# Kernel optimization log

Measured on AMD Instinct MI355X. Metric: run time of the kernel, lower is better.

## Reference

```python
import jax, jax.numpy as jnp
import numpy as np

OUT_F, IN_F, BLOCK, RANK = 8192, 8192, 32, 16
B, S = 4, 256
Q_ZERO = 128.0      # symmetric int8-style zero point for the Q8_0-like quants
LORA_SCALE = 2.0    # patch alpha applied by the patch function


def setup_inputs() -> dict:
    key = jax.random.key(0)
    k1, k2, k3, k4, k5, k6 = jax.random.split(key, 6)
    x = jax.random.normal(k1, (B, S, IN_F), dtype=jnp.float32)
    # block-quantized weight: int quants in [0,256) and per-block scales
    q_int = jax.random.randint(k2, (OUT_F, IN_F // BLOCK, BLOCK), 0, 256, dtype=jnp.int32)
    scales = jax.random.uniform(k3, (OUT_F, IN_F // BLOCK), dtype=jnp.float32) * 0.02
    lora_A = jax.random.normal(k4, (RANK, IN_F), dtype=jnp.float32) * 0.02
    lora_B = jax.random.normal(k5, (OUT_F, RANK), dtype=jnp.float32) * 0.02
    bias = jax.random.normal(k6, (OUT_F,), dtype=jnp.float32)
    return {"x": x, "q_int": q_int, "scales": scales,
            "lora_A": lora_A, "lora_B": lora_B, "bias": bias}


def reference(x, q_int, scales, lora_A, lora_B, bias):
    # --- get_weight(): dequantize GGML block-quantized tensor ---
    # w[o, b, e] = (q[o, b, e] - 128) * scale[o, b]
    w = (q_int.astype(jnp.float32) - Q_ZERO) * scales[:, :, None]   # [out, in//BLOCK, BLOCK]
    w = w.reshape(OUT_F, IN_F)                                      # [out, in]
    # --- apply patch function (LoRA add) ---
    w = w + LORA_SCALE * (lora_B @ lora_A)                          # [out, in]
    # --- cast_bias_weight + F.linear ---
    w = w.astype(x.dtype)
    y = jnp.einsum('bsi,oi->bso', x, w) + bias.astype(x.dtype)      # [B, S, out]
    return y
```

## Files before the change

kernel.cpp:

```cpp
#include <hip/hip_runtime.h>
#include <hip/hip_bf16.h>
#include <stdint.h>

#define OUT_F 8192
#define IN_F  8192
#define RANK  16
#define M_TOT 1024
#define BM 128
#define BN 128
#define BK 64
#define NK (IN_F / BK)
#define SCB (IN_F / 32)

typedef __bf16 bf16x8 __attribute__((ext_vector_type(8)));
typedef float  f32x4  __attribute__((ext_vector_type(4)));

static __device__ __forceinline__ uint32_t pack_bf16(float lo, float hi) {
    uint32_t a = __builtin_bit_cast(uint32_t, lo);
    uint32_t b = __builtin_bit_cast(uint32_t, hi);
    return ((a + 0x8000u) >> 16) | ((b + 0x8000u) & 0xffff0000u);
}

__global__ __launch_bounds__(256) void prep_kernel(
    const float* __restrict__ x, const int* __restrict__ q,
    uint2* __restrict__ xb2, uint32_t* __restrict__ qu32,
    float* __restrict__ t)
{
    const int gid = blockIdx.x * 256 + threadIdx.x;
    if (gid < M_TOT * RANK) t[gid] = 0.f;

    const float4* x4 = (const float4*)x;
#pragma unroll
    for (int j = 0; j < 4; ++j) {
        const int i = gid + j * 524288;
        const float4 v = x4[i];
        uint2 p;
        p.x = pack_bf16(v.x, v.y);
        p.y = pack_bf16(v.z, v.w);
        xb2[i] = p;
    }

    const int4* q4 = (const int4*)q;
#pragma unroll 8
    for (int k = 0; k < 32; ++k) {
        const size_t i = (size_t)gid + (size_t)k * 524288;
        const int4 a = q4[i];
        qu32[i] = (uint32_t)a.x | ((uint32_t)a.y << 8) |
                  ((uint32_t)a.z << 16) | ((uint32_t)a.w << 24);
    }
}

__global__ __launch_bounds__(256) void convert_kernel(
    const float* __restrict__ x, uint2* __restrict__ xb2, float* __restrict__ t)
{
    const int tid = threadIdx.x, b = blockIdx.x;
    if (b < 64) t[b * 256 + tid] = 0.f;
    const float4* x4 = (const float4*)x;
    const int base = b * 256 + tid;
#pragma unroll
    for (int j = 0; j < 8; ++j) {
        const int i = base + j * 262144;
        const float4 v = x4[i];
        uint2 p;
        p.x = pack_bf16(v.x, v.y);
        p.y = pack_bf16(v.z, v.w);
        xb2[i] = p;
    }
}

__global__ __launch_bounds__(256) void lora_t_kernel(
    const uint16_t* __restrict__ xb, const float* __restrict__ lora_A,
    float* __restrict__ t)
{
    const int b = blockIdx.x;
    const int mt = b >> 6, ks = b & 63;
    const int tid = threadIdx.x, wave = tid >> 6, lane = tid & 63;
    const int fr = lane & 15, quad = lane >> 4;
    const int m = mt * 64 + wave * 16 + fr;
    const int k0 = ks * 128 + quad * 8;

    f32x4 acc = {0.f, 0.f, 0.f, 0.f};
    const uint16_t* xr = xb + (size_t)m * IN_F + k0;
    const float* ar = lora_A + (size_t)fr * IN_F + k0;

#pragma unroll
    for (int s = 0; s < 4; ++s) {
        const bf16x8 af = *(const bf16x8*)(xr + s * 32);
        const float4 a0 = *(const float4*)(ar + s * 32);
        const float4 a1 = *(const float4*)(ar + s * 32 + 4);
        bf16x8 bfr;
        uint32_t* bp = (uint32_t*)&bfr;
        bp[0] = pack_bf16(a0.x, a0.y); bp[1] = pack_bf16(a0.z, a0.w);
        bp[2] = pack_bf16(a1.x, a1.y); bp[3] = pack_bf16(a1.z, a1.w);
        acc = __builtin_amdgcn_mfma_f32_16x16x32_bf16(af, bfr, acc, 0, 0, 0);
    }
    const int mout = mt * 64 + wave * 16 + quad * 4;
#pragma unroll
    for (int r = 0; r < 4; ++r)
        atomicAdd(&t[(size_t)(mout + r) * RANK + fr], acc[r]);
}

#define GEMM_STEP_U(KT, P, CUR, NXT)                                           \
    {                                                                          \
        const int ktn = ((KT) + 2) & (NK - 1);                                 \
        _Pragma("unroll")                                                      \
        for (int j = 0; j < 8; ++j) {                                          \
            const int row = qrow + 16 * j;                                     \
            qv[(P) ^ 1][j] = *(const uint32_t*)(qbase + (size_t)row * IN_F + ktn * BK); \
            sc[(P) ^ 1][j] = scales[(size_t)(n0 + row) * SCB + ktn * 2 + qhi]; \
        }                                                                      \
        const int kta = ((KT) + 1) & (NK - 1);                                 \
        _Pragma("unroll")                                                      \
        for (int i = 0; i < 4; ++i) {                                          \
            __builtin_amdgcn_global_load_lds(                                  \
                (const __attribute__((address_space(1))) uint32_t*)(xsrc + (size_t)kta * BK + (size_t)i * 8 * IN_F), \
                (__attribute__((address_space(3))) uint32_t*)(&xs[NXT][(wave * 32 + i * 8) * BK]), \
                16, 0, 0);                                                     \
        }                                                                      \
        _Pragma("unroll")                                                      \
        for (int j = 0; j < 8; ++j) {                                          \
            const float s = sc[P][j];                                          \
            const float c = -128.f * s;                                        \
            const uint32_t qq = qv[P][j];                                      \
            uint2 pk;                                                          \
            pk.x = pack_bf16(fmaf((float)(qq & 0xffu), s, c),                  \
                             fmaf((float)((qq >> 8) & 0xffu), s, c));          \
            pk.y = pack_bf16(fmaf((float)((qq >> 16) & 0xffu), s, c),          \
                             fmaf((float)(qq >> 24), s, c));                   \
            *(uint2*)(&wt[NXT][(qrow + 16 * j) * BK + wpos]) = pk;             \
        }                                                                      \
        _Pragma("unroll")                                                      \
        for (int kk = 0; kk < BK; kk += 32) {                                  \
            bf16x8 af[4], bfr[4];                                              \
            const int pp = (((kk >> 3) + quad) ^ (fr & 7)) * 8;                \
            _Pragma("unroll")                                                  \
            for (int i = 0; i < 4; ++i)                                        \
                af[i] = *(const bf16x8*)(&xs[CUR][(wm * 64 + i * 16 + fr) * BK + pp]); \
            _Pragma("unroll")                                                  \
            for (int j = 0; j < 4; ++j)                                        \
                bfr[j] = *(const bf16x8*)(&wt[CUR][(wn * 64 + j * 16 + fr) * BK + pp]); \
            _Pragma("unroll")                                                  \
            for (int i = 0; i < 4; ++i)                                        \
                _Pragma("unroll")                                              \
                for (int j = 0; j < 4; ++j)                                    \
                    acc[i][j] = __builtin_amdgcn_mfma_f32_16x16x32_bf16(af[i], bfr[j], acc[i][j], 0, 0, 0); \
        }                                                                      \
        __syncthreads();                                                       \
    }

__global__ __launch_bounds__(256, 2) void gemm_u8_kernel(
    const uint16_t* __restrict__ xb,
    const uint8_t*  __restrict__ qu8,
    const float*    __restrict__ scales,
    const float*    __restrict__ t,
    const float*    __restrict__ loraB,
    const float*    __restrict__ bias,
    float*          __restrict__ out)
{
    __shared__ __align__(16) uint16_t xs[2][BM * BK];
    __shared__ __align__(16) uint16_t wt[2][BN * BK];

    const int bx    = blockIdx.x;
    const int mtile = bx >> 6;
    const int ntile = bx & 63;
    const int m0 = mtile * BM;
    const int n0 = ntile * BN;

    const int tid  = threadIdx.x;
    const int wave = tid >> 6;
    const int lane = tid & 63;
    const int wm = wave & 1, wn = wave >> 1;
    const int fr = lane & 15;
    const int quad = lane >> 4;

    const int qrow  = tid >> 4;
    const int qcol4 = (tid & 15) * 4;
    const int qhi   = (tid >> 3) & 1;
    const int wpos = ((((tid >> 1) & 7) ^ (qrow & 7)) * 8) + (tid & 1) * 4;

    const uint8_t* qbase = qu8 + (size_t)n0 * IN_F + qcol4;

    f32x4 acc[4][4];
    const f32x4 z = {0.f, 0.f, 0.f, 0.f};
#pragma unroll
    for (int i = 0; i < 4; ++i)
#pragma unroll
        for (int j = 0; j < 4; ++j) acc[i][j] = z;

    uint32_t qv[2][8];
    float    sc[2][8];

#pragma unroll
    for (int j = 0; j < 8; ++j) {
        const int row = qrow + 16 * j;
        qv[0][j] = *(const uint32_t*)(qbase + (size_t)row * IN_F);
        sc[0][j] = scales[(size_t)(n0 + row) * SCB + qhi];
    }

    {
        if (tid < 128) {
            const int row = tid, s = row & 7;
            const float4* tp = (const float4*)(t + (size_t)(m0 + row) * RANK);
            const float4 v0 = tp[0], v1 = tp[1], v2 = tp[2], v3 = tp[3];
            uint32_t vals[8];
            vals[0] = pack_bf16(v0.x, v0.y); vals[1] = pack_bf16(v0.z, v0.w);
            vals[2] = pack_bf16(v1.x, v1.y); vals[3] = pack_bf16(v1.z, v1.w);
            vals[4] = pack_bf16(v2.x, v2.y); vals[5] = pack_bf16(v2.z, v2.w);
            vals[6] = pack_bf16(v3.x, v3.y); vals[7] = pack_bf16(v3.z, v3.w);
            uint32_t* dst = (uint32_t*)(&xs[0][row * BK]);
#pragma unroll
            for (int c = 0; c < 8; ++c) {
                const int p = (c ^ s) * 4;
                if (c < 2) {
                    dst[p + 0] = vals[c * 4 + 0]; dst[p + 1] = vals[c * 4 + 1];
                    dst[p + 2] = vals[c * 4 + 2]; dst[p + 3] = vals[c * 4 + 3];
                } else {
                    dst[p + 0] = 0; dst[p + 1] = 0; dst[p + 2] = 0; dst[p + 3] = 0;
                }
            }
        } else {
            const int row = tid - 128, s = row & 7;
            const float4* bp = (const float4*)(loraB + (size_t)(n0 + row) * RANK);
            const float4 v0 = bp[0], v1 = bp[1], v2 = bp[2], v3 = bp[3];
            uint32_t vals[8];
            vals[0] = pack_bf16(2.f * v0.x, 2.f * v0.y); vals[1] = pack_bf16(2.f * v0.z, 2.f * v0.w);
            vals[2] = pack_bf16(2.f * v1.x, 2.f * v1.y); vals[3] = pack_bf16(2.f * v1.z, 2.f * v1.w);
            vals[4] = pack_bf16(2.f * v2.x, 2.f * v2.y); vals[5] = pack_bf16(2.f * v2.z, 2.f * v2.w);
            vals[6] = pack_bf16(2.f * v3.x, 2.f * v3.y); vals[7] = pack_bf16(2.f * v3.z, 2.f * v3.w);
            uint32_t* dst = (uint32_t*)(&wt[0][row * BK]);
#pragma unroll
            for (int c = 0; c < 8; ++c) {
                const int p = (c ^ s) * 4;
                if (c < 2) {
                    dst[p + 0] = vals[c * 4 + 0]; dst[p + 1] = vals[c * 4 + 1];
                    dst[p + 2] = vals[c * 4 + 2]; dst[p + 3] = vals[c * 4 + 3];
                } else {
                    dst[p + 0] = 0; dst[p + 1] = 0; dst[p + 2] = 0; dst[p + 3] = 0;
                }
            }
        }
        __syncthreads();
        const int pp = (quad ^ (fr & 7)) * 8;
        bf16x8 af[4], bfr[4];
#pragma unroll
        for (int i = 0; i < 4; ++i)
            af[i] = *(const bf16x8*)(&xs[0][(wm * 64 + i * 16 + fr) * BK + pp]);
#pragma unroll
        for (int j = 0; j < 4; ++j)
            bfr[j] = *(const bf16x8*)(&wt[0][(wn * 64 + j * 16 + fr) * BK + pp]);
#pragma unroll
        for (int i = 0; i < 4; ++i)
#pragma unroll
            for (int j = 0; j < 4; ++j)
                acc[i][j] = __builtin_amdgcn_mfma_f32_16x16x32_bf16(af[i], bfr[j], acc[i][j], 0, 0, 0);
        __syncthreads();
    }

    const int xrow   = wave * 32 + (lane >> 3);
    const int xchunk = (lane & 7) ^ (lane >> 3);
    const uint16_t* xsrc = xb + (size_t)(m0 + xrow) * IN_F + xchunk * 8;

#pragma unroll
    for (int i = 0; i < 4; ++i) {
        __builtin_amdgcn_global_load_lds(
            (const __attribute__((address_space(1))) uint32_t*)(xsrc + (size_t)i * 8 * IN_F),
            (__attribute__((address_space(3))) uint32_t*)(&xs[0][(wave * 32 + i * 8) * BK]),
            16, 0, 0);
    }
#pragma unroll
    for (int j = 0; j < 8; ++j) {
        const float s = sc[0][j];
        const float c = -128.f * s;
        const uint32_t qq = qv[0][j];
        uint2 pk;
        pk.x = pack_bf16(fmaf((float)(qq & 0xffu), s, c),
                         fmaf((float)((qq >> 8) & 0xffu), s, c));
        pk.y = pack_bf16(fmaf((float)((qq >> 16) & 0xffu), s, c),
                         fmaf((float)(qq >> 24), s, c));
        *(uint2*)(&wt[0][(qrow + 16 * j) * BK + wpos]) = pk;
    }
#pragma unroll
    for (int j = 0; j < 8; ++j) {
        const int row = qrow + 16 * j;
        qv[0][j] = *(const uint32_t*)(qbase + (size_t)row * IN_F + 1 * BK);
        sc[0][j] = scales[(size_t)(n0 + row) * SCB + 2 + qhi];
    }
    __syncthreads();

    for (int kt = 0; kt < NK; kt += 2) {
        GEMM_STEP_U(kt,     0, 0, 1);
        GEMM_STEP_U(kt + 1, 1, 1, 0);
    }

#pragma unroll
    for (int j = 0; j < 4; ++j) {
        const int col = n0 + wn * 64 + j * 16 + fr;
        const float bv = bias[col];
#pragma unroll
        for (int i = 0; i < 4; ++i) {
            const int rbase = m0 + wm * 64 + i * 16 + quad * 4;
#pragma unroll
            for (int r = 0; r < 4; ++r)
                out[(size_t)(rbase + r) * OUT_F + col] = acc[i][j][r] + bv;
        }
    }
}

#define GEMM_STEP_L(KT, P, CUR, NXT)                                           \
    {                                                                          \
        const int ktn = ((KT) + 2) & (NK - 1);                                 \
        _Pragma("unroll")                                                      \
        for (int j = 0; j < 8; ++j) {                                          \
            const int row = qrow + 16 * j;                                     \
            qv[(P) ^ 1][j] = *(const int4*)(qbase + (size_t)row * IN_F + ktn * BK); \
            sc[(P) ^ 1][j] = scales[(size_t)(n0 + row) * SCB + ktn * 2 + qhi]; \
        }                                                                      \
        const int kta = ((KT) + 1) & (NK - 1);                                 \
        _Pragma("unroll")                                                      \
        for (int i = 0; i < 4; ++i) {                                          \
            __builtin_amdgcn_global_load_lds(                                  \
                (const __attribute__((address_space(1))) uint32_t*)(xsrc + (size_t)kta * BK + (size_t)i * 8 * IN_F), \
                (__attribute__((address_space(3))) uint32_t*)(&xs[NXT][(wave * 32 + i * 8) * BK]), \
                16, 0, 0);                                                     \
        }                                                                      \
        _Pragma("unroll")                                                      \
        for (int j = 0; j < 8; ++j) {                                          \
            const float s = sc[P][j];                                          \
            const float c = -128.f * s;                                        \
            const int4 qq = qv[P][j];                                          \
            uint2 pk;                                                          \
            pk.x = pack_bf16(fmaf((float)qq.x, s, c), fmaf((float)qq.y, s, c)); \
            pk.y = pack_bf16(fmaf((float)qq.z, s, c), fmaf((float)qq.w, s, c)); \
            *(uint2*)(&wt[NXT][(qrow + 16 * j) * BK + wpos]) = pk;             \
        }                                                                      \
        _Pragma("unroll")                                                      \
        for (int kk = 0; kk < BK; kk += 32) {                                  \
            bf16x8 af[4], bfr[4];                                              \
            const int pp = (((kk >> 3) + quad) ^ (fr & 7)) * 8;                \
            _Pragma("unroll")                                                  \
            for (int i = 0; i < 4; ++i)                                        \
                af[i] = *(const bf16x8*)(&xs[CUR][(wm * 64 + i * 16 + fr) * BK + pp]); \
            _Pragma("unroll")                                                  \
            for (int j = 0; j < 4; ++j)                                        \
                bfr[j] = *(const bf16x8*)(&wt[CUR][(wn * 64 + j * 16 + fr) * BK + pp]); \
            _Pragma("unroll")                                                  \
            for (int i = 0; i < 4; ++i)                                        \
                _Pragma("unroll")                                              \
                for (int j = 0; j < 4; ++j)                                    \
                    acc[i][j] = __builtin_amdgcn_mfma_f32_16x16x32_bf16(af[i], bfr[j], acc[i][j], 0, 0, 0); \
        }                                                                      \
        __syncthreads();                                                       \
    }

__global__ __launch_bounds__(256, 2) void gemm_kernel(
    const uint16_t* __restrict__ xb,
    const int*      __restrict__ q,
    const float*    __restrict__ scales,
    const float*    __restrict__ t,
    const float*    __restrict__ loraB,
    const float*    __restrict__ bias,
    float*          __restrict__ out)
{
    __shared__ __align__(16) uint16_t xs[2][BM * BK];
    __shared__ __align__(16) uint16_t wt[2][BN * BK];

    const int bx    = blockIdx.x;
    const int mtile = bx >> 6;
    const int ntile = bx & 63;
    const int m0 = mtile * BM;
    const int n0 = ntile * BN;

    const int tid  = threadIdx.x;
    const int wave = tid >> 6;
    const int lane = tid & 63;
    const int wm = wave & 1, wn = wave >> 1;
    const int fr = lane & 15;
    const int quad = lane >> 4;

    const int qrow  = tid >> 4;
    const int qcol4 = (tid & 15) * 4;
    const int qhi   = (tid >> 3) & 1;
    const int wpos = ((((tid >> 1) & 7) ^ (qrow & 7)) * 8) + (tid & 1) * 4;

    const int* qbase = q + (size_t)n0 * IN_F + qcol4;

    f32x4 acc[4][4];
    const f32x4 z = {0.f, 0.f, 0.f, 0.f};
#pragma unroll
    for (int i = 0; i < 4; ++i)
#pragma unroll
        for (int j = 0; j < 4; ++j) acc[i][j] = z;

    int4  qv[2][8];
    float sc[2][8];

#pragma unroll
    for (int j = 0; j < 8; ++j) {
        const int row = qrow + 16 * j;
        qv[0][j] = *(const int4*)(qbase + (size_t)row * IN_F);
        sc[0][j] = scales[(size_t)(n0 + row) * SCB + qhi];
    }

    {
        if (tid < 128) {
            const int row = tid, s = row & 7;
            const float4* tp = (const float4*)(t + (size_t)(m0 + row) * RANK);
            const float4 v0 = tp[0], v1 = tp[1], v2 = tp[2], v3 = tp[3];
            uint32_t vals[8];
            vals[0] = pack_bf16(v0.x, v0.y); vals[1] = pack_bf16(v0.z, v0.w);
            vals[2] = pack_bf16(v1.x, v1.y); vals[3] = pack_bf16(v1.z, v1.w);
            vals[4] = pack_bf16(v2.x, v2.y); vals[5] = pack_bf16(v2.z, v2.w);
            vals[6] = pack_bf16(v3.x, v3.y); vals[7] = pack_bf16(v3.z, v3.w);
            uint32_t* dst = (uint32_t*)(&xs[0][row * BK]);
#pragma unroll
            for (int c = 0; c < 8; ++c) {
                const int p = (c ^ s) * 4;
                if (c < 2) {
                    dst[p + 0] = vals[c * 4 + 0]; dst[p + 1] = vals[c * 4 + 1];
                    dst[p + 2] = vals[c * 4 + 2]; dst[p + 3] = vals[c * 4 + 3];
                } else {
                    dst[p + 0] = 0; dst[p + 1] = 0; dst[p + 2] = 0; dst[p + 3] = 0;
                }
            }
        } else {
            const int row = tid - 128, s = row & 7;
            const float4* bp = (const float4*)(loraB + (size_t)(n0 + row) * RANK);
            const float4 v0 = bp[0], v1 = bp[1], v2 = bp[2], v3 = bp[3];
            uint32_t vals[8];
            vals[0] = pack_bf16(2.f * v0.x, 2.f * v0.y); vals[1] = pack_bf16(2.f * v0.z, 2.f * v0.w);
            vals[2] = pack_bf16(2.f * v1.x, 2.f * v1.y); vals[3] = pack_bf16(2.f * v1.z, 2.f * v1.w);
            vals[4] = pack_bf16(2.f * v2.x, 2.f * v2.y); vals[5] = pack_bf16(2.f * v2.z, 2.f * v2.w);
            vals[6] = pack_bf16(2.f * v3.x, 2.f * v3.y); vals[7] = pack_bf16(2.f * v3.z, 2.f * v3.w);
            uint32_t* dst = (uint32_t*)(&wt[0][row * BK]);
#pragma unroll
            for (int c = 0; c < 8; ++c) {
                const int p = (c ^ s) * 4;
                if (c < 2) {
                    dst[p + 0] = vals[c * 4 + 0]; dst[p + 1] = vals[c * 4 + 1];
                    dst[p + 2] = vals[c * 4 + 2]; dst[p + 3] = vals[c * 4 + 3];
                } else {
                    dst[p + 0] = 0; dst[p + 1] = 0; dst[p + 2] = 0; dst[p + 3] = 0;
                }
            }
        }
        __syncthreads();
        const int pp = (quad ^ (fr & 7)) * 8;
        bf16x8 af[4], bfr[4];
#pragma unroll
        for (int i = 0; i < 4; ++i)
            af[i] = *(const bf16x8*)(&xs[0][(wm * 64 + i * 16 + fr) * BK + pp]);
#pragma unroll
        for (int j = 0; j < 4; ++j)
            bfr[j] = *(const bf16x8*)(&wt[0][(wn * 64 + j * 16 + fr) * BK + pp]);
#pragma unroll
        for (int i = 0; i < 4; ++i)
#pragma unroll
            for (int j = 0; j < 4; ++j)
                acc[i][j] = __builtin_amdgcn_mfma_f32_16x16x32_bf16(af[i], bfr[j], acc[i][j], 0, 0, 0);
        __syncthreads();
    }

    const int xrow   = wave * 32 + (lane >> 3);
    const int xchunk = (lane & 7) ^ (lane >> 3);
    const uint16_t* xsrc = xb + (size_t)(m0 + xrow) * IN_F + xchunk * 8;

#pragma unroll
    for (int i = 0; i < 4; ++i) {
        __builtin_amdgcn_global_load_lds(
            (const __attribute__((address_space(1))) uint32_t*)(xsrc + (size_t)i * 8 * IN_F),
            (__attribute__((address_space(3))) uint32_t*)(&xs[0][(wave * 32 + i * 8) * BK]),
            16, 0, 0);
    }
#pragma unroll
    for (int j = 0; j < 8; ++j) {
        const float s = sc[0][j];
        const float c = -128.f * s;
        const int4 qq = qv[0][j];
        uint2 pk;
        pk.x = pack_bf16(fmaf((float)qq.x, s, c), fmaf((float)qq.y, s, c));
        pk.y = pack_bf16(fmaf((float)qq.z, s, c), fmaf((float)qq.w, s, c));
        *(uint2*)(&wt[0][(qrow + 16 * j) * BK + wpos]) = pk;
    }
#pragma unroll
    for (int j = 0; j < 8; ++j) {
        const int row = qrow + 16 * j;
        qv[0][j] = *(const int4*)(qbase + (size_t)row * IN_F + 1 * BK);
        sc[0][j] = scales[(size_t)(n0 + row) * SCB + 2 + qhi];
    }
    __syncthreads();

    for (int kt = 0; kt < NK; kt += 2) {
        GEMM_STEP_L(kt,     0, 0, 1);
        GEMM_STEP_L(kt + 1, 1, 1, 0);
    }

#pragma unroll
    for (int j = 0; j < 4; ++j) {
        const int col = n0 + wn * 64 + j * 16 + fr;
        const float bv = bias[col];
#pragma unroll
        for (int i = 0; i < 4; ++i) {
            const int rbase = m0 + wm * 64 + i * 16 + quad * 4;
#pragma unroll
            for (int r = 0; r < 4; ++r)
                out[(size_t)(rbase + r) * OUT_F + col] = acc[i][j][r] + bv;
        }
    }
}

extern "C" void kernel_launch(void* const* d_in, const int* in_sizes, int n_in,
                              void* d_out, int out_size, void* d_ws, size_t ws_size,
                              hipStream_t stream) {
    const float* x      = (const float*)d_in[0];
    const int*   q      = (const int*)d_in[1];
    const float* scales = (const float*)d_in[2];
    const float* lora_A = (const float*)d_in[3];
    const float* lora_B = (const float*)d_in[4];
    const float* bias   = (const float*)d_in[5];
    float* out = (float*)d_out;

    const size_t xb_bytes = (size_t)M_TOT * IN_F * sizeof(uint16_t);
    const size_t t_bytes  = (size_t)M_TOT * RANK * sizeof(float);
    const size_t q8_off   = xb_bytes + t_bytes;
    const size_t q8_bytes = (size_t)OUT_F * IN_F;

    uint16_t* xb = (uint16_t*)d_ws;
    float*    t  = (float*)((char*)d_ws + xb_bytes);

    if (ws_size >= q8_off + q8_bytes) {
        uint8_t* qu8 = (uint8_t*)d_ws + q8_off;
        prep_kernel<<<2048, 256, 0, stream>>>(x, q, (uint2*)xb, (uint32_t*)qu8, t);
        lora_t_kernel<<<1024, 256, 0, stream>>>(xb, lora_A, t);
        gemm_u8_kernel<<<(M_TOT / BM) * (OUT_F / BN), 256, 0, stream>>>(
            xb, qu8, scales, t, lora_B, bias, out);
    } else {
        convert_kernel<<<M_TOT, 256, 0, stream>>>(x, (uint2*)xb, t);
        lora_t_kernel<<<1024, 256, 0, stream>>>(xb, lora_A, t);
        gemm_kernel<<<(M_TOT / BM) * (OUT_F / BN), 256, 0, stream>>>(
            xb, q, scales, t, lora_B, bias, out);
    }
}
```

Baseline: 602.3 us.

## Split K in two with single-buffered LDS, higher occupancy, and a reduce kernel

Adds a split-K GEMM that gives each of 1024 workgroups half of the K range and writes fp32 partial tiles to a workspace buffer. A separate reduce kernel then adds the two partials and the bias. The new kernel uses single-buffered LDS with launch bounds of 4 blocks per CU, trading the double-buffered pipeline for more resident waves and a 1024-block grid on the CUs. The cost is an extra 64 MB of partial traffic plus a reduce pass. It also drops the old int32 fallback path and needs a larger workspace to take the new path.

```diff
diff --git a/kernel.cpp b/kernel.cpp
--- a/kernel.cpp
+++ b/kernel.cpp
@@ -98,6 +98,207 @@
 #pragma unroll
     for (int r = 0; r < 4; ++r)
         atomicAdd(&t[(size_t)(mout + r) * RANK + fr], acc[r]);
+}
+
+#define GEMM_STEP_S(KT, KTN, P)                                                \
+    {                                                                          \
+        _Pragma("unroll")                                                      \
+        for (int i = 0; i < 4; ++i) {                                          \
+            __builtin_amdgcn_global_load_lds(                                  \
+                (const __attribute__((address_space(1))) uint32_t*)(xsrc + (size_t)(KT) * BK + (size_t)i * 8 * IN_F), \
+                (__attribute__((address_space(3))) uint32_t*)(&xs[(wave * 32 + i * 8) * BK]), \
+                16, 0, 0);                                                     \
+        }                                                                      \
+        _Pragma("unroll")                                                      \
+        for (int j = 0; j < 8; ++j) {                                          \
+            const float s = sc[P][j];                                          \
+            const float c = -128.f * s;                                        \
+            const uint32_t qq = qv[P][j];                                      \
+            uint2 pk;                                                          \
+            pk.x = pack_bf16(fmaf((float)(qq & 0xffu), s, c),                  \
+                             fmaf((float)((qq >> 8) & 0xffu), s, c));          \
+            pk.y = pack_bf16(fmaf((float)((qq >> 16) & 0xffu), s, c),          \
+                             fmaf((float)(qq >> 24), s, c));                   \
+            *(uint2*)(&wt[(qrow + 16 * j) * BK + wpos]) = pk;                  \
+        }                                                                      \
+        _Pragma("unroll")                                                      \
+        for (int j = 0; j < 8; ++j) {                                          \
+            const int row = qrow + 16 * j;                                     \
+            qv[(P) ^ 1][j] = *(const uint32_t*)(qbase + (size_t)row * IN_F + (size_t)(KTN) * BK); \
+            sc[(P) ^ 1][j] = scales[(size_t)(n0 + row) * SCB + (KTN) * 2 + qhi]; \
+        }                                                                      \
+        __syncthreads();   \
+        _Pragma("unroll")                                                      \
+        for (int kk = 0; kk < BK; kk += 32) {                                  \
+            bf16x8 af[4], bfr[4];                                              \
+            const int pp = (((kk >> 3) + quad) ^ (fr & 7)) * 8;                \
+            _Pragma("unroll")                                                  \
+            for (int i = 0; i < 4; ++i)                                        \
+                af[i] = *(const bf16x8*)(&xs[(wm * 64 + i * 16 + fr) * BK + pp]); \
+            _Pragma("unroll")                                                  \
+            for (int j = 0; j < 4; ++j)                                        \
+                bfr[j] = *(const bf16x8*)(&wt[(wn * 64 + j * 16 + fr) * BK + pp]); \
+            _Pragma("unroll")                                                  \
+            for (int i = 0; i < 4; ++i)                                        \
+                _Pragma("unroll")                                              \
+                for (int j = 0; j < 4; ++j)                                    \
+                    acc[i][j] = __builtin_amdgcn_mfma_f32_16x16x32_bf16(af[i], bfr[j], acc[i][j], 0, 0, 0); \
+        }                                                                      \
+        __syncthreads();                       \
+    }
+
+__global__ __launch_bounds__(256, 4) void gemm_u8s_kernel(
+    const uint16_t* __restrict__ xb,
+    const uint8_t*  __restrict__ qu8,
+    const float*    __restrict__ scales,
+    const float*    __restrict__ t,
+    const float*    __restrict__ loraB,
+    float*          __restrict__ part)
+{
+    __shared__ __align__(16) uint16_t xs[BM * BK];
+    __shared__ __align__(16) uint16_t wt[BN * BK];
+
+    const int bx    = blockIdx.x;
+    const int ks    = bx >> 9;
+    const int mtile = (bx >> 6) & 7;
+    const int ntile = bx & 63;
+    const int m0 = mtile * BM;
+    const int n0 = ntile * BN;
+    const int k0 = ks * (NK / 2);
+
+    const int tid  = threadIdx.x;
+    const int wave = tid >> 6;
+    const int lane = tid & 63;
+    const int wm = wave & 1, wn = wave >> 1;
+    const int fr = lane & 15;
+    const int quad = lane >> 4;
+
+    const int qrow  = tid >> 4;
+    const int qcol4 = (tid & 15) * 4;
+    const int qhi   = (tid >> 3) & 1;
+    const int wpos = ((((tid >> 1) & 7) ^ (qrow & 7)) * 8) + (tid & 1) * 4;
+
+    const uint8_t* qbase = qu8 + (size_t)n0 * IN_F + qcol4;
+
+    f32x4 acc[4][4];
+    const f32x4 z = {0.f, 0.f, 0.f, 0.f};
+#pragma unroll
+    for (int i = 0; i < 4; ++i)
+#pragma unroll
+        for (int j = 0; j < 4; ++j) acc[i][j] = z;
+
+    uint32_t qv[2][8];
+    float    sc[2][8];
+
+#pragma unroll
+    for (int j = 0; j < 8; ++j) {
+        const int row = qrow + 16 * j;
+        qv[0][j] = *(const uint32_t*)(qbase + (size_t)row * IN_F + (size_t)k0 * BK);
+        sc[0][j] = scales[(size_t)(n0 + row) * SCB + k0 * 2 + qhi];
+    }
+
+    if (ks == 0) {
+        if (tid < 128) {
+            const int row = tid, s = row & 7;
+            const float4* tp = (const float4*)(t + (size_t)(m0 + row) * RANK);
+            const float4 v0 = tp[0], v1 = tp[1], v2 = tp[2], v3 = tp[3];
+            uint32_t vals[8];
+            vals[0] = pack_bf16(v0.x, v0.y); vals[1] = pack_bf16(v0.z, v0.w);
+            vals[2] = pack_bf16(v1.x, v1.y); vals[3] = pack_bf16(v1.z, v1.w);
+            vals[4] = pack_bf16(v2.x, v2.y); vals[5] = pack_bf16(v2.z, v2.w);
+            vals[6] = pack_bf16(v3.x, v3.y); vals[7] = pack_bf16(v3.z, v3.w);
+            uint32_t* dst = (uint32_t*)(&xs[row * BK]);
+#pragma unroll
+            for (int c = 0; c < 8; ++c) {
+                const int p = (c ^ s) * 4;
+                if (c < 2) {
+                    dst[p + 0] = vals[c * 4 + 0]; dst[p + 1] = vals[c * 4 + 1];
+                    dst[p + 2] = vals[c * 4 + 2]; dst[p + 3] = vals[c * 4 + 3];
+                } else {
+                    dst[p + 0] = 0; dst[p + 1] = 0; dst[p + 2] = 0; dst[p + 3] = 0;
+                }
+            }
+        } else {
+            const int row = tid - 128, s = row & 7;
+            const float4* bp = (const float4*)(loraB + (size_t)(n0 + row) * RANK);
+            const float4 v0 = bp[0], v1 = bp[1], v2 = bp[2], v3 = bp[3];
+            uint32_t vals[8];
+            vals[0] = pack_bf16(2.f * v0.x, 2.f * v0.y); vals[1] = pack_bf16(2.f * v0.z, 2.f * v0.w);
+            vals[2] = pack_bf16(2.f * v1.x, 2.f * v1.y); vals[3] = pack_bf16(2.f * v1.z, 2.f * v1.w);
+            vals[4] = pack_bf16(2.f * v2.x, 2.f * v2.y); vals[5] = pack_bf16(2.f * v2.z, 2.f * v2.w);
+            vals[6] = pack_bf16(2.f * v3.x, 2.f * v3.y); vals[7] = pack_bf16(2.f * v3.z, 2.f * v3.w);
+            uint32_t* dst = (uint32_t*)(&wt[row * BK]);
+#pragma unroll
+            for (int c = 0; c < 8; ++c) {
+                const int p = (c ^ s) * 4;
+                if (c < 2) {
+                    dst[p + 0] = vals[c * 4 + 0]; dst[p + 1] = vals[c * 4 + 1];
+                    dst[p + 2] = vals[c * 4 + 2]; dst[p + 3] = vals[c * 4 + 3];
+                } else {
+                    dst[p + 0] = 0; dst[p + 1] = 0; dst[p + 2] = 0; dst[p + 3] = 0;
+                }
+            }
+        }
+        __syncthreads();
+        const int pp = (quad ^ (fr & 7)) * 8;
+        bf16x8 af[4], bfr[4];
+#pragma unroll
+        for (int i = 0; i < 4; ++i)
+            af[i] = *(const bf16x8*)(&xs[(wm * 64 + i * 16 + fr) * BK + pp]);
+#pragma unroll
+        for (int j = 0; j < 4; ++j)
+            bfr[j] = *(const bf16x8*)(&wt[(wn * 64 + j * 16 + fr) * BK + pp]);
+#pragma unroll
+        for (int i = 0; i < 4; ++i)
+#pragma unroll
+            for (int j = 0; j < 4; ++j)
+                acc[i][j] = __builtin_amdgcn_mfma_f32_16x16x32_bf16(af[i], bfr[j], acc[i][j], 0, 0, 0);
+        __syncthreads();
+    }
+
+    const int xrow   = wave * 32 + (lane >> 3);
+    const int xchunk = (lane & 7) ^ (lane >> 3);
+    const uint16_t* xsrc = xb + (size_t)(m0 + xrow) * IN_F + xchunk * 8;
+
+    for (int lt = 0; lt < NK / 2; lt += 2) {
+        const int kt = k0 + lt;
+        GEMM_STEP_S(kt,     k0 + ((lt + 1) & (NK / 2 - 1)), 0);
+        GEMM_STEP_S(kt + 1, k0 + ((lt + 2) & (NK / 2 - 1)), 1);
+    }
+
+    float* pdst = part + (size_t)ks * M_TOT * OUT_F;
+#pragma unroll
+    for (int j = 0; j < 4; ++j) {
+        const int col = n0 + wn * 64 + j * 16 + fr;
+#pragma unroll
+        for (int i = 0; i < 4; ++i) {
+            const int rbase = m0 + wm * 64 + i * 16 + quad * 4;
+#pragma unroll
+            for (int r = 0; r < 4; ++r)
+                pdst[(size_t)(rbase + r) * OUT_F + col] = acc[i][j][r];
+        }
+    }
+}
+
+__global__ __launch_bounds__(256) void reduce_kernel(
+    const float4* __restrict__ p, const float* __restrict__ bias,
+    float4* __restrict__ out4)
+{
+    const int idx = blockIdx.x * 256 + threadIdx.x;
+    const float4* b4 = (const float4*)bias;
+#pragma unroll
+    for (int j = 0; j < 4; ++j) {
+        const int f = idx + j * 524288;
+        const float4 a = p[f];
+        const float4 b = p[f + 2097152];
+        const float4 bv = b4[f & 2047];
+        float4 o;
+        o.x = a.x + b.x + bv.x;
+        o.y = a.y + b.y + bv.y;
+        o.z = a.z + b.z + bv.z;
+        o.w = a.w + b.w + bv.w;
+        out4[f] = o;
+    }
 }
 
 #define GEMM_STEP_U(KT, P, CUR, NXT)                                           \
@@ -306,208 +507,6 @@
     }
 }
 
-#define GEMM_STEP_L(KT, P, CUR, NXT)                                           \
-    {                                                                          \
-        const int ktn = ((KT) + 2) & (NK - 1);                                 \
-        _Pragma("unroll")                                                      \
-        for (int j = 0; j < 8; ++j) {                                          \
-            const int row = qrow + 16 * j;                                     \
-            qv[(P) ^ 1][j] = *(const int4*)(qbase + (size_t)row * IN_F + ktn * BK); \
-            sc[(P) ^ 1][j] = scales[(size_t)(n0 + row) * SCB + ktn * 2 + qhi]; \
-        }                                                                      \
-        const int kta = ((KT) + 1) & (NK - 1);                                 \
-        _Pragma("unroll")                                                      \
-        for (int i = 0; i < 4; ++i) {                                          \
-            __builtin_amdgcn_global_load_lds(                                  \
-                (const __attribute__((address_space(1))) uint32_t*)(xsrc + (size_t)kta * BK + (size_t)i * 8 * IN_F), \
-                (__attribute__((address_space(3))) uint32_t*)(&xs[NXT][(wave * 32 + i * 8) * BK]), \
-                16, 0, 0);                                                     \
-        }                                                                      \
-        _Pragma("unroll")                                                      \
-        for (int j = 0; j < 8; ++j) {                                          \
-            const float s = sc[P][j];                                          \
-            const float c = -128.f * s;                                        \
-            const int4 qq = qv[P][j];                                          \
-            uint2 pk;                                                          \
-            pk.x = pack_bf16(fmaf((float)qq.x, s, c), fmaf((float)qq.y, s, c)); \
-            pk.y = pack_bf16(fmaf((float)qq.z, s, c), fmaf((float)qq.w, s, c)); \
-            *(uint2*)(&wt[NXT][(qrow + 16 * j) * BK + wpos]) = pk;             \
-        }                                                                      \
-        _Pragma("unroll")                                                      \
-        for (int kk = 0; kk < BK; kk += 32) {                                  \
-            bf16x8 af[4], bfr[4];                                              \
-            const int pp = (((kk >> 3) + quad) ^ (fr & 7)) * 8;                \
-            _Pragma("unroll")                                                  \
-            for (int i = 0; i < 4; ++i)                                        \
-                af[i] = *(const bf16x8*)(&xs[CUR][(wm * 64 + i * 16 + fr) * BK + pp]); \
-            _Pragma("unroll")                                                  \
-            for (int j = 0; j < 4; ++j)                                        \
-                bfr[j] = *(const bf16x8*)(&wt[CUR][(wn * 64 + j * 16 + fr) * BK + pp]); \
-            _Pragma("unroll")                                                  \
-            for (int i = 0; i < 4; ++i)                                        \
-                _Pragma("unroll")                                              \
-                for (int j = 0; j < 4; ++j)                                    \
-                    acc[i][j] = __builtin_amdgcn_mfma_f32_16x16x32_bf16(af[i], bfr[j], acc[i][j], 0, 0, 0); \
-        }                                                                      \
-        __syncthreads();                                                       \
-    }
-
-__global__ __launch_bounds__(256, 2) void gemm_kernel(
-    const uint16_t* __restrict__ xb,
-    const int*      __restrict__ q,
-    const float*    __restrict__ scales,
-    const float*    __restrict__ t,
-    const float*    __restrict__ loraB,
-    const float*    __restrict__ bias,
-    float*          __restrict__ out)
-{
-    __shared__ __align__(16) uint16_t xs[2][BM * BK];
-    __shared__ __align__(16) uint16_t wt[2][BN * BK];
-
-    const int bx    = blockIdx.x;
-    const int mtile = bx >> 6;
-    const int ntile = bx & 63;
-    const int m0 = mtile * BM;
-    const int n0 = ntile * BN;
-
-    const int tid  = threadIdx.x;
-    const int wave = tid >> 6;
-    const int lane = tid & 63;
-    const int wm = wave & 1, wn = wave >> 1;
-    const int fr = lane & 15;
-    const int quad = lane >> 4;
-
-    const int qrow  = tid >> 4;
-    const int qcol4 = (tid & 15) * 4;
-    const int qhi   = (tid >> 3) & 1;
-    const int wpos = ((((tid >> 1) & 7) ^ (qrow & 7)) * 8) + (tid & 1) * 4;
-
-    const int* qbase = q + (size_t)n0 * IN_F + qcol4;
-
-    f32x4 acc[4][4];
-    const f32x4 z = {0.f, 0.f, 0.f, 0.f};
-#pragma unroll
-    for (int i = 0; i < 4; ++i)
-#pragma unroll
-        for (int j = 0; j < 4; ++j) acc[i][j] = z;
-
-    int4  qv[2][8];
-    float sc[2][8];
-
-#pragma unroll
-    for (int j = 0; j < 8; ++j) {
-        const int row = qrow + 16 * j;
-        qv[0][j] = *(const int4*)(qbase + (size_t)row * IN_F);
-        sc[0][j] = scales[(size_t)(n0 + row) * SCB + qhi];
-    }
-
-    {
-        if (tid < 128) {
-            const int row = tid, s = row & 7;
-            const float4* tp = (const float4*)(t + (size_t)(m0 + row) * RANK);
-            const float4 v0 = tp[0], v1 = tp[1], v2 = tp[2], v3 = tp[3];
-            uint32_t vals[8];
-            vals[0] = pack_bf16(v0.x, v0.y); vals[1] = pack_bf16(v0.z, v0.w);
-            vals[2] = pack_bf16(v1.x, v1.y); vals[3] = pack_bf16(v1.z, v1.w);
-            vals[4] = pack_bf16(v2.x, v2.y); vals[5] = pack_bf16(v2.z, v2.w);
-            vals[6] = pack_bf16(v3.x, v3.y); vals[7] = pack_bf16(v3.z, v3.w);
-            uint32_t* dst = (uint32_t*)(&xs[0][row * BK]);
-#pragma unroll
-            for (int c = 0; c < 8; ++c) {
-                const int p = (c ^ s) * 4;
-                if (c < 2) {
-                    dst[p + 0] = vals[c * 4 + 0]; dst[p + 1] = vals[c * 4 + 1];
-                    dst[p + 2] = vals[c * 4 + 2]; dst[p + 3] = vals[c * 4 + 3];
-                } else {
-                    dst[p + 0] = 0; dst[p + 1] = 0; dst[p + 2] = 0; dst[p + 3] = 0;
-                }
-            }
-        } else {
-            const int row = tid - 128, s = row & 7;
-            const float4* bp = (const float4*)(loraB + (size_t)(n0 + row) * RANK);
-            const float4 v0 = bp[0], v1 = bp[1], v2 = bp[2], v3 = bp[3];
-            uint32_t vals[8];
-            vals[0] = pack_bf16(2.f * v0.x, 2.f * v0.y); vals[1] = pack_bf16(2.f * v0.z, 2.f * v0.w);
-            vals[2] = pack_bf16(2.f * v1.x, 2.f * v1.y); vals[3] = pack_bf16(2.f * v1.z, 2.f * v1.w);
-            vals[4] = pack_bf16(2.f * v2.x, 2.f * v2.y); vals[5] = pack_bf16(2.f * v2.z, 2.f * v2.w);
-            vals[6] = pack_bf16(2.f * v3.x, 2.f * v3.y); vals[7] = pack_bf16(2.f * v3.z, 2.f * v3.w);
-            uint32_t* dst = (uint32_t*)(&wt[0][row * BK]);
-#pragma unroll
-            for (int c = 0; c < 8; ++c) {
-                const int p = (c ^ s) * 4;
-                if (c < 2) {
-                    dst[p + 0] = vals[c * 4 + 0]; dst[p + 1] = vals[c * 4 + 1];
-                    dst[p + 2] = vals[c * 4 + 2]; dst[p + 3] = vals[c * 4 + 3];
-                } else {
-                    dst[p + 0] = 0; dst[p + 1] = 0; dst[p + 2] = 0; dst[p + 3] = 0;
-                }
-            }
-        }
-        __syncthreads();
-        const int pp = (quad ^ (fr & 7)) * 8;
-        bf16x8 af[4], bfr[4];
-#pragma unroll
-        for (int i = 0; i < 4; ++i)
-            af[i] = *(const bf16x8*)(&xs[0][(wm * 64 + i * 16 + fr) * BK + pp]);
-#pragma unroll
-        for (int j = 0; j < 4; ++j)
-            bfr[j] = *(const bf16x8*)(&wt[0][(wn * 64 + j * 16 + fr) * BK + pp]);
-#pragma unroll
-        for (int i = 0; i < 4; ++i)
-#pragma unroll
-            for (int j = 0; j < 4; ++j)
-                acc[i][j] = __builtin_amdgcn_mfma_f32_16x16x32_bf16(af[i], bfr[j], acc[i][j], 0, 0, 0);
-        __syncthreads();
-    }
-
-    const int xrow   = wave * 32 + (lane >> 3);
-    const int xchunk = (lane & 7) ^ (lane >> 3);
-    const uint16_t* xsrc = xb + (size_t)(m0 + xrow) * IN_F + xchunk * 8;
-
-#pragma unroll
-    for (int i = 0; i < 4; ++i) {
-        __builtin_amdgcn_global_load_lds(
-            (const __attribute__((address_space(1))) uint32_t*)(xsrc + (size_t)i * 8 * IN_F),
-            (__attribute__((address_space(3))) uint32_t*)(&xs[0][(wave * 32 + i * 8) * BK]),
-            16, 0, 0);
-    }
-#pragma unroll
-    for (int j = 0; j < 8; ++j) {
-        const float s = sc[0][j];
-        const float c = -128.f * s;
-        const int4 qq = qv[0][j];
-        uint2 pk;
-        pk.x = pack_bf16(fmaf((float)qq.x, s, c), fmaf((float)qq.y, s, c));
-        pk.y = pack_bf16(fmaf((float)qq.z, s, c), fmaf((float)qq.w, s, c));
-        *(uint2*)(&wt[0][(qrow + 16 * j) * BK + wpos]) = pk;
-    }
-#pragma unroll
-    for (int j = 0; j < 8; ++j) {
-        const int row = qrow + 16 * j;
-        qv[0][j] = *(const int4*)(qbase + (size_t)row * IN_F + 1 * BK);
-        sc[0][j] = scales[(size_t)(n0 + row) * SCB + 2 + qhi];
-    }
-    __syncthreads();
-
-    for (int kt = 0; kt < NK; kt += 2) {
-        GEMM_STEP_L(kt,     0, 0, 1);
-        GEMM_STEP_L(kt + 1, 1, 1, 0);
-    }
-
-#pragma unroll
-    for (int j = 0; j < 4; ++j) {
-        const int col = n0 + wn * 64 + j * 16 + fr;
-        const float bv = bias[col];
-#pragma unroll
-        for (int i = 0; i < 4; ++i) {
-            const int rbase = m0 + wm * 64 + i * 16 + quad * 4;
-#pragma unroll
-            for (int r = 0; r < 4; ++r)
-                out[(size_t)(rbase + r) * OUT_F + col] = acc[i][j][r] + bv;
-        }
-    }
-}
-
 extern "C" void kernel_launch(void* const* d_in, const int* in_sizes, int n_in,
                               void* d_out, int out_size, void* d_ws, size_t ws_size,
                               hipStream_t stream) {
@@ -523,20 +522,25 @@
     const size_t t_bytes  = (size_t)M_TOT * RANK * sizeof(float);
     const size_t q8_off   = xb_bytes + t_bytes;
     const size_t q8_bytes = (size_t)OUT_F * IN_F;
+    const size_t p_off    = q8_off + q8_bytes;
+    const size_t p_bytes  = (size_t)2 * M_TOT * OUT_F * sizeof(float);
 
     uint16_t* xb = (uint16_t*)d_ws;
     float*    t  = (float*)((char*)d_ws + xb_bytes);
 
-    if (ws_size >= q8_off + q8_bytes) {
+    if (ws_size >= p_off + p_bytes) {
+        uint8_t* qu8  = (uint8_t*)d_ws + q8_off;
+        float*   part = (float*)((char*)d_ws + p_off);
+        prep_kernel<<<2048, 256, 0, stream>>>(x, q, (uint2*)xb, (uint32_t*)qu8, t);
+        lora_t_kernel<<<1024, 256, 0, stream>>>(xb, lora_A, t);
+        gemm_u8s_kernel<<<2 * (M_TOT / BM) * (OUT_F / BN), 256, 0, stream>>>(
+            xb, qu8, scales, t, lora_B, part);
+        reduce_kernel<<<2048, 256, 0, stream>>>((const float4*)part, bias, (float4*)out);
+    } else {
         uint8_t* qu8 = (uint8_t*)d_ws + q8_off;
         prep_kernel<<<2048, 256, 0, stream>>>(x, q, (uint2*)xb, (uint32_t*)qu8, t);
         lora_t_kernel<<<1024, 256, 0, stream>>>(xb, lora_A, t);
         gemm_u8_kernel<<<(M_TOT / BM) * (OUT_F / BN), 256, 0, stream>>>(
             xb, qu8, scales, t, lora_B, bias, out);
-    } else {
-        convert_kernel<<<M_TOT, 256, 0, stream>>>(x, (uint2*)xb, t);
-        lora_t_kernel<<<1024, 256, 0, stream>>>(xb, lora_A, t);
-        gemm_kernel<<<(M_TOT / BM) * (OUT_F / BN), 256, 0, stream>>>(
-            xb, q, scales, t, lora_B, bias, out);
-    }
-}
+    }
+}
```

Result: slower. 1.402 ms (+132.7%).
